# Performance work log

Hardware: AMD Instinct MI355X
Metric: run time of the kernel (lower is better)

Reference implementation:

```python
import jax, jax.numpy as jnp
import numpy as np

B = 2048   # batch
C = 64     # EEG channels (num_eegch)
T = 125    # time samples -> pool5 -> 25 -> (p=5, 5)
H = 8      # num_heads
L = 6      # num_layers
D = 16     # num_projected_features
QK = 8     # qkv_len
P = 5      # tokens before cls
EPS = 1e-5


def setup_inputs() -> dict:
    key = jax.random.key(0)
    ks = iter(jax.random.split(key, 64))

    def nrm(shape, s=0.05):
        return jax.random.normal(next(ks), shape, jnp.float32) * s

    return {
        "x": jax.random.normal(next(ks), (B, 1, C, T), jnp.float32),
        "conv_t_w": nrm((8, 1, 1, 63)),
        "conv_t_b": nrm((8,)),
        "bn1_g": 1.0 + nrm((8,)),
        "bn1_b": nrm((8,)),
        "bn1_m": nrm((8,)),
        "bn1_v": 1.0 + 0.1 * jax.random.uniform(next(ks), (8,), jnp.float32),
        "conv_s_w": nrm((16, 1, C, 1)),
        "conv_s_b": nrm((16,)),
        "bn2_g": 1.0 + nrm((16,)),
        "bn2_b": nrm((16,)),
        "bn2_m": nrm((16,)),
        "bn2_v": 1.0 + 0.1 * jax.random.uniform(next(ks), (16,), jnp.float32),
        "proj_w": nrm((D, 16 * 5)),
        "proj_b": nrm((D,)),
        "cls_token": nrm((1, 1, D), 1.0),
        "pe": nrm((1, P + 1, D), 1.0),
        "qkv_w": nrm((L, 3 * H * QK, D)),
        "qkv_b": nrm((L, 3 * H * QK)),
        "out_w": nrm((L, D, H * QK)),
        "out_b": nrm((L, D)),
        "ln1_g": jnp.ones((L, D), jnp.float32),
        "ln1_b": jnp.zeros((L, D), jnp.float32),
        "ln2_g": jnp.ones((L, D), jnp.float32),
        "ln2_b": jnp.zeros((L, D), jnp.float32),
        "mlp_w1": nrm((L, 2 * D, D)),
        "mlp_b1": nrm((L, 2 * D)),
        "mlp_w2": nrm((L, D, 2 * D)),
        "mlp_b2": nrm((L, D)),
        "head_ln_g": jnp.ones((D,), jnp.float32),
        "head_ln_b": jnp.zeros((D,), jnp.float32),
        "head_w": nrm((2, D)),
        "head_b": nrm((2,)),
    }


def _bn(z, g, b, m, v):
    s = (g * jax.lax.rsqrt(v + EPS))[None, :, None, None]
    return (z - m[None, :, None, None]) * s + b[None, :, None, None]


def _ln(z, g, b):
    m = z.mean(-1, keepdims=True)
    var = jnp.mean((z - m) ** 2, -1, keepdims=True)
    return (z - m) * jax.lax.rsqrt(var + EPS) * g + b


def _forward(x, conv_t_w, conv_t_b, bn1_g, bn1_b, bn1_m, bn1_v,
             conv_s_w, conv_s_b, bn2_g, bn2_b, bn2_m, bn2_v,
             proj_w, proj_b, cls_token, pe,
             qkv_w, qkv_b, out_w, out_b, ln1_g, ln1_b, ln2_g, ln2_b,
             mlp_w1, mlp_b1, mlp_w2, mlp_b2,
             head_ln_g, head_ln_b, head_w, head_b):
    b = x.shape[0]
    dn = ('NCHW', 'OIHW', 'NCHW')
    # temporal conv, 'same' padding on width (kernel 63 -> pad 31/31)
    y = jax.lax.conv_general_dilated(x, conv_t_w, (1, 1), [(0, 0), (31, 31)], dimension_numbers=dn)
    y = _bn(y + conv_t_b[None, :, None, None], bn1_g, bn1_b, bn1_m, bn1_v)
    # grouped spatial conv collapses the EEG-channel axis
    y = jax.lax.conv_general_dilated(y, conv_s_w, (1, 1), 'VALID', dimension_numbers=dn, feature_group_count=8)
    y = _bn(y + conv_s_b[None, :, None, None], bn2_g, bn2_b, bn2_m, bn2_v)
    y = jax.nn.elu(y)                              # (b,16,1,125)
    y = y.reshape(b, 16, 1, T // 5, 5).mean(-1)    # avg_pool2d (1,5) -> (b,16,1,25)
    # dropout: identity at inference
    y = y.reshape(b, 16, 1, P, 5)
    y = jnp.swapaxes(y, 3, 4)
    tok = jnp.swapaxes(y.reshape(b, 16 * 5, P), 1, 2)   # (b,5,80)
    tok = tok @ proj_w.T + proj_b                       # (b,5,16)
    z = jnp.concatenate([jnp.broadcast_to(cls_token, (b, 1, D)), tok], axis=1) + pe  # (b,6,16)
    scale = QK ** -0.5
    for i in range(L):
        h1 = _ln(z, ln1_g[i], ln1_b[i])
        qkv = h1 @ qkv_w[i].T + qkv_b[i]                # (b,6,3*H*QK)
        q, k, v = jnp.split(qkv, 3, axis=-1)
        q = q.reshape(b, P + 1, H, QK).transpose(0, 2, 1, 3)
        k = k.reshape(b, P + 1, H, QK).transpose(0, 2, 1, 3)
        v = v.reshape(b, P + 1, H, QK).transpose(0, 2, 1, 3)
        att = jax.nn.softmax(jnp.einsum('bhsd,bhtd->bhst', q, k) * scale, axis=-1)
        o = jnp.einsum('bhst,bhtd->bhsd', att, v).transpose(0, 2, 1, 3).reshape(b, P + 1, H * QK)
        z = o @ out_w[i].T + out_b[i] + z
        h2 = _ln(z, ln2_g[i], ln2_b[i])
        m = jax.nn.gelu(h2 @ mlp_w1[i].T + mlp_b1[i], approximate=False) @ mlp_w2[i].T + mlp_b2[i]
        z = m + z
    cls = _ln(z[:, 0, :], head_ln_g, head_ln_b)
    return jax.nn.softmax(cls @ head_w.T + head_b, axis=-1)


def reference(x, conv_t_w, conv_t_b, bn1_g, bn1_b, bn1_m, bn1_v,
              conv_s_w, conv_s_b, bn2_g, bn2_b, bn2_m, bn2_v,
              proj_w, proj_b, cls_token, pe,
              qkv_w, qkv_b, out_w, out_b, ln1_g, ln1_b, ln2_g, ln2_b,
              mlp_w1, mlp_b1, mlp_w2, mlp_b2,
              head_ln_g, head_ln_b, head_w, head_b):
    return _forward(x, conv_t_w, conv_t_b, bn1_g, bn1_b, bn1_m, bn1_v,
                    conv_s_w, conv_s_b, bn2_g, bn2_b, bn2_m, bn2_v,
                    proj_w, proj_b, cls_token, pe,
                    qkv_w, qkv_b, out_w, out_b, ln1_g, ln1_b, ln2_g, ln2_b,
                    mlp_w1, mlp_b1, mlp_w2, mlp_b2,
                    head_ln_g, head_ln_b, head_w, head_b)
```

## Files before the change

kernel.cpp:

```cpp
#include <hip/hip_runtime.h>

#define WAVE_SYNC() do { asm volatile("" ::: "memory"); \
                         __builtin_amdgcn_wave_barrier(); \
                         asm volatile("" ::: "memory"); } while (0)

typedef _Float16 h2 __attribute__((ext_vector_type(2)));
typedef _Float16 h4 __attribute__((ext_vector_type(4)));
typedef _Float16 h8 __attribute__((ext_vector_type(8)));

__device__ __forceinline__ float fdot2(h2 a, h2 b, float c) {
#if defined(__has_builtin)
#if __has_builtin(__builtin_amdgcn_fdot2)
    return __builtin_amdgcn_fdot2(a, b, c, false);
#else
    return (float)a[0]*(float)b[0] + (float)a[1]*(float)b[1] + c;
#endif
#else
    return (float)a[0]*(float)b[0] + (float)a[1]*(float)b[1] + c;
#endif
}

__device__ __forceinline__ float dot8h(h8 a, h8 b, float c) {
    float s = c;
    #pragma unroll
    for (int i = 0; i < 4; ++i) {
        h2 x = {a[2*i], a[2*i+1]};
        h2 y = {b[2*i], b[2*i+1]};
        s = fdot2(x, y, s);
    }
    return s;
}

__device__ __forceinline__ float dot16h(h8 a0, h8 a1, h8 b0, h8 b1, float c) {
    return dot8h(a1, b1, dot8h(a0, b0, c));
}

__device__ __forceinline__ float ln_norm16(float z, float g, float bb) {
    float s = z, q = z * z;
    #pragma unroll
    for (int off = 8; off >= 1; off >>= 1) {
        s += __shfl_xor(s, off, 16);
        q += __shfl_xor(q, off, 16);
    }
    float mean = s * 0.0625f;
    float var  = q * 0.0625f - mean * mean;
    return (z - mean) * rsqrtf(var + 1e-5f) * g + bb;
}

__device__ __forceinline__ float gelu_exact(float a) {
    float xa = fabsf(a) * 0.70710678118654752f;
    float tt = 1.f / (1.f + 0.3275911f * xa);
    float poly = tt * (0.254829592f + tt * (-0.284496736f + tt * (1.421413741f
               + tt * (-1.453152027f + tt * 1.061405429f))));
    float erfv = 1.f - poly * __expf(-xa * xa);
    erfv = a >= 0.f ? erfv : -erfv;
    return 0.5f * a * (1.f + erfv);
}

#define F_XSTR 204
#define F_PL   4000
#define F_TOT  4448

extern "C" __global__ __launch_bounds__(64, 2)
void eegnet_frontend(
    const float* __restrict__ x,
    const float* __restrict__ conv_t_w, const float* __restrict__ conv_t_b,
    const float* __restrict__ bn1_g, const float* __restrict__ bn1_b,
    const float* __restrict__ bn1_m, const float* __restrict__ bn1_v,
    const float* __restrict__ conv_s_w, const float* __restrict__ conv_s_b,
    const float* __restrict__ bn2_g, const float* __restrict__ bn2_b,
    const float* __restrict__ bn2_m, const float* __restrict__ bn2_v,
    const float* __restrict__ proj_w, const float* __restrict__ proj_b,
    float* __restrict__ tokws)
{
    __shared__ __align__(16) float sm[F_TOT];
    _Float16* xr = reinterpret_cast<_Float16*>(sm);
    const int b    = blockIdx.x;
    const int lane = threadIdx.x;

    {
        const float4* xb4 = reinterpret_cast<const float4*>(x + (size_t)b * 8000);
        #pragma unroll
        for (int k = 0; k < 32; ++k) {
            int g = min(k * 64 + lane, 1999);
            float4 v = xb4[g];
            h4 hv = {(_Float16)v.x, (_Float16)v.y, (_Float16)v.z, (_Float16)v.w};
            *reinterpret_cast<h4*>(&xr[4 * g]) = hv;
        }
    }
    WAVE_SYNC();

    {
        const int l2 = min(lane, 60);
        float a0[16], a1[16];
        #pragma unroll
        for (int o = 0; o < 16; ++o) { a0[o] = 0.f; a1[o] = 0.f; }
        #pragma unroll 8
        for (int c = 0; c < 64; ++c) {
            float xv0 = (float)xr[c * 125 + lane];
            float xv1 = (float)xr[c * 125 + 64 + l2];
            #pragma unroll
            for (int o = 0; o < 16; ++o) {
                float w = conv_s_w[o * 64 + c];
                a0[o] += w * xv0;
                a1[o] += w * xv1;
            }
        }
        WAVE_SYNC();

        for (int i = lane; i < 16 * 79; i += 64) {
            int row = i / 79, k = i - row * 79;
            int off = (k < 32) ? k : (k + 125);
            sm[row * F_XSTR + off] = 0.f;
        }
        #pragma unroll
        for (int o = 0; o < 16; ++o) {
            sm[o * F_XSTR + 32 + lane] = a0[o];
            if (lane < 61) sm[o * F_XSTR + 96 + lane] = a1[o];
        }
    }

    const int oo = lane & 15, qg = lane >> 4, gg = oo >> 1;
    float sa, cc;
    {
        float s1 = bn1_g[gg] * rsqrtf(bn1_v[gg] + 1e-5f);
        float b1 = (conv_t_b[gg] - bn1_m[gg]) * s1 + bn1_b[gg];
        float s2 = bn2_g[oo] * rsqrtf(bn2_v[oo] + 1e-5f);
        float ssum = 0.f;
        const float4* csw = reinterpret_cast<const float4*>(conv_s_w + oo * 64);
        #pragma unroll
        for (int i = 0; i < 16; ++i) {
            float4 v = csw[i];
            ssum += v.x + v.y + v.z + v.w;
        }
        sa = s1 * s2;
        cc = (b1 * ssum + conv_s_b[oo] - bn2_m[oo]) * s2 + bn2_b[oo];
    }
    float wt[63];
    #pragma unroll
    for (int k = 0; k < 63; ++k) wt[k] = conv_t_w[gg * 63 + k];

    WAVE_SYNC();

    #pragma unroll 2
    for (int jj = 0; jj < 7; ++jj) {
        int j  = qg * 7 + jj;
        int jc = min(j, 24);
        int base = oo * F_XSTR + 5 * jc + 1;
        float acc5[5] = {0.f, 0.f, 0.f, 0.f, 0.f};
        #pragma unroll
        for (int m = 0; m < 67; ++m) {
            float xv = sm[base + m];
            #pragma unroll
            for (int u = 0; u < 5; ++u)
                if (u <= m && m - u <= 62) acc5[u] += wt[m - u] * xv;
        }
        float psum = 0.f;
        #pragma unroll
        for (int u = 0; u < 5; ++u) {
            float v = acc5[u] * sa + cc;
            psum += (v > 0.f) ? v : (__expf(v) - 1.f);
        }
        if (j == jc) sm[F_PL + oo * 28 + j] = psum * 0.2f;
    }

    WAVE_SYNC();

    #pragma unroll
    for (int pass = 0; pass < 2; ++pass) {
        int oi = (pass == 0) ? lane : (64 + lane);
        int p = oi >> 4, dd = oi & 15;
        int pc = min(p, 4);
        bool act = (pass == 0) || (lane < 16);
        float acc = proj_b[dd];
        const float4* wp = reinterpret_cast<const float4*>(proj_w + dd * 80);
        #pragma unroll
        for (int i = 0; i < 20; ++i) {
            float4 w4 = wp[i];
            acc += w4.x * sm[F_PL + ((4*i+0)/5) * 28 + pc * 5 + ((4*i+0)%5)];
            acc += w4.y * sm[F_PL + ((4*i+1)/5) * 28 + pc * 5 + ((4*i+1)%5)];
            acc += w4.z * sm[F_PL + ((4*i+2)/5) * 28 + pc * 5 + ((4*i+2)%5)];
            acc += w4.w * sm[F_PL + ((4*i+3)/5) * 28 + pc * 5 + ((4*i+3)%5)];
        }
        if (act) tokws[b * 80 + pc * 16 + dd] = acc;
    }
}

#define WQKVH 0
#define WOUTH 4608
#define WM1H  5760
#define WM2H  6528
#define BQKVF 3584
#define BOUTF 3776
#define BM1F  3792
#define BM2F  3824
#define LN1GF 3840
#define LN1BF 3856
#define LN2GF 3872
#define LN2BF 3888
#define SCR0  7808
#define SSTRH 1584
#define SH1H  0
#define SQKVH 144
#define SMHSH 1344
#define T_BYTES 28288

extern "C" __global__ __launch_bounds__(256, 2)
void eegnet_transformer(
    const float* __restrict__ cls_token, const float* __restrict__ pe,
    const float* __restrict__ qkv_w, const float* __restrict__ qkv_b,
    const float* __restrict__ out_w, const float* __restrict__ out_b,
    const float* __restrict__ ln1_g, const float* __restrict__ ln1_b,
    const float* __restrict__ ln2_g, const float* __restrict__ ln2_b,
    const float* __restrict__ mlp_w1, const float* __restrict__ mlp_b1,
    const float* __restrict__ mlp_w2, const float* __restrict__ mlp_b2,
    const float* __restrict__ head_ln_g, const float* __restrict__ head_ln_b,
    const float* __restrict__ head_w, const float* __restrict__ head_b,
    const float* __restrict__ tokws, float* __restrict__ out)
{
    __shared__ __align__(16) unsigned char smb[T_BYTES];
    float*    smf = reinterpret_cast<float*>(smb);
    _Float16* smh = reinterpret_cast<_Float16*>(smb);

    const int tid = threadIdx.x;
    const int ss  = tid >> 7;
    const int u   = tid & 127;
    const int sA  = blockIdx.x * 4 + ss * 2;
    const int d16 = u & 15, qg = u >> 4;
    const int t6c = min(qg, 5);
    const int wav = u >> 6, al = u & 63;
    const int sbA = SCR0 + (ss * 2    ) * SSTRH;
    const int sbB = SCR0 + (ss * 2 + 1) * SSTRH;

    float zA, zB;
    {
        float peV = pe[t6c * 16 + d16];
        if (t6c == 0) {
            float cv = cls_token[d16];
            zA = cv + peV; zB = cv + peV;
        } else {
            zA = tokws[(sA    ) * 80 + (t6c - 1) * 16 + d16] + peV;
            zB = tokws[(sA + 1) * 80 + (t6c - 1) * 16 + d16] + peV;
        }
    }

    #pragma unroll 1
    for (int li = 0; li < 6; ++li) {
        __syncthreads();

        {
            const float4* s1 = reinterpret_cast<const float4*>(qkv_w + li * 3072);
            #pragma unroll
            for (int it = 0; it < 3; ++it) {
                int i = tid + it * 256;
                float4 v = s1[i];
                int j = i >> 2, k = (i & 3) << 2;
                h4 hv = {(_Float16)v.x, (_Float16)v.y, (_Float16)v.z, (_Float16)v.w};
                *reinterpret_cast<h4*>(&smh[WQKVH + j * 24 + k]) = hv;
            }
            {
                float4 v = reinterpret_cast<const float4*>(out_w + li * 1024)[tid];
                int j = tid >> 4, k = (tid & 15) << 2;
                h4 hv = {(_Float16)v.x, (_Float16)v.y, (_Float16)v.z, (_Float16)v.w};
                *reinterpret_cast<h4*>(&smh[WOUTH + j * 72 + k]) = hv;
            }
            if (tid < 128) {
                float4 v = reinterpret_cast<const float4*>(mlp_w1 + li * 512)[tid];
                int j = tid >> 2, k = (tid & 3) << 2;
                h4 hv = {(_Float16)v.x, (_Float16)v.y, (_Float16)v.z, (_Float16)v.w};
                *reinterpret_cast<h4*>(&smh[WM1H + j * 24 + k]) = hv;
            } else {
                int i = tid - 128;
                float4 v = reinterpret_cast<const float4*>(mlp_w2 + li * 512)[i];
                int j = i >> 3, k = (i & 7) << 2;
                h4 hv = {(_Float16)v.x, (_Float16)v.y, (_Float16)v.z, (_Float16)v.w};
                *reinterpret_cast<h4*>(&smh[WM2H + j * 40 + k]) = hv;
            }
            if (tid < 192) smf[BQKVF + tid] = qkv_b[li * 192 + tid];
            else if (tid < 208) smf[BOUTF + tid - 192] = out_b[li * 16 + tid - 192];
            else if (tid < 240) smf[BM1F + tid - 208]  = mlp_b1[li * 32 + tid - 208];
            else               smf[BM2F + tid - 240]  = mlp_b2[li * 16 + tid - 240];
            if (tid >= 64 && tid < 80)        smf[LN1GF + tid - 64]  = ln1_g[li * 16 + tid - 64];
            else if (tid >= 80 && tid < 96)   smf[LN1BF + tid - 80]  = ln1_b[li * 16 + tid - 80];
            else if (tid >= 96 && tid < 112)  smf[LN2GF + tid - 96]  = ln2_g[li * 16 + tid - 96];
            else if (tid >= 112 && tid < 128) smf[LN2BF + tid - 112] = ln2_b[li * 16 + tid - 112];
        }
        __syncthreads();

        {
            float g = smf[LN1GF + d16], bb = smf[LN1BF + d16];
            smh[sbA + SH1H + t6c * 24 + d16] = (_Float16)ln_norm16(zA, g, bb);
            smh[sbB + SH1H + t6c * 24 + d16] = (_Float16)ln_norm16(zB, g, bb);
        }
        WAVE_SYNC();

        h8 hA0 = *reinterpret_cast<const h8*>(&smh[sbA + SH1H + t6c * 24]);
        h8 hA1 = *reinterpret_cast<const h8*>(&smh[sbA + SH1H + t6c * 24 + 8]);
        h8 hB0 = *reinterpret_cast<const h8*>(&smh[sbB + SH1H + t6c * 24]);
        h8 hB1 = *reinterpret_cast<const h8*>(&smh[sbB + SH1H + t6c * 24 + 8]);

        #pragma unroll 2
        for (int r = 0; r < 12; ++r) {
            int j = d16 + 16 * r;
            h8 w0 = *reinterpret_cast<const h8*>(&smh[WQKVH + j * 24]);
            h8 w1 = *reinterpret_cast<const h8*>(&smh[WQKVH + j * 24 + 8]);
            float bb = smf[BQKVF + j];
            smh[sbA + SQKVH + t6c * 200 + j] = (_Float16)dot16h(hA0, hA1, w0, w1, bb);
            smh[sbB + SQKVH + t6c * 200 + j] = (_Float16)dot16h(hB0, hB1, w0, w1, bb);
        }
        __syncthreads();

        {
            bool act = (wav == 0) ? (al < 32) : (al < 16);
            if (act) {
                int h  = al & 7;
                int qs = (wav == 0) ? (al >> 3) : 4 + (al >> 3);
                const int qoffA = sbA + SQKVH + qs * 200 + h * 8;
                const int qoffB = sbB + SQKVH + qs * 200 + h * 8;
                h8 qA = *reinterpret_cast<const h8*>(&smh[qoffA]);
                h8 qB = *reinterpret_cast<const h8*>(&smh[qoffB]);
                float scA[6], scB[6];
                #pragma unroll
                for (int t = 0; t < 6; ++t) {
                    h8 kA = *reinterpret_cast<const h8*>(&smh[sbA + SQKVH + t * 200 + 64 + h * 8]);
                    h8 kB = *reinterpret_cast<const h8*>(&smh[sbB + SQKVH + t * 200 + 64 + h * 8]);
                    scA[t] = dot8h(qA, kA, 0.f) * 0.35355339059327373f;
                    scB[t] = dot8h(qB, kB, 0.f) * 0.35355339059327373f;
                }
                float mxA = scA[0], mxB = scB[0];
                #pragma unroll
                for (int t = 1; t < 6; ++t) { mxA = fmaxf(mxA, scA[t]); mxB = fmaxf(mxB, scB[t]); }
                float suA = 0.f, suB = 0.f;
                #pragma unroll
                for (int t = 0; t < 6; ++t) {
                    scA[t] = __expf(scA[t] - mxA); suA += scA[t];
                    scB[t] = __expf(scB[t] - mxB); suB += scB[t];
                }
                float ivA = 1.f / suA, ivB = 1.f / suB;
                h2 oA[4], oB[4];
                #pragma unroll
                for (int k2 = 0; k2 < 4; ++k2) { oA[k2] = h2{0, 0}; oB[k2] = h2{0, 0}; }
                #pragma unroll
                for (int t = 0; t < 6; ++t) {
                    h8 vA = *reinterpret_cast<const h8*>(&smh[sbA + SQKVH + t * 200 + 128 + h * 8]);
                    h8 vB = *reinterpret_cast<const h8*>(&smh[sbB + SQKVH + t * 200 + 128 + h * 8]);
                    _Float16 aa = (_Float16)(scA[t] * ivA);
                    _Float16 ab = (_Float16)(scB[t] * ivB);
                    h2 av = {aa, aa}, bv = {ab, ab};
                    #pragma unroll
                    for (int k2 = 0; k2 < 4; ++k2) {
                        h2 va = {vA[2*k2], vA[2*k2+1]};
                        h2 vb = {vB[2*k2], vB[2*k2+1]};
                        oA[k2] += av * va;
                        oB[k2] += bv * vb;
                    }
                }
                h8 stA, stB;
                #pragma unroll
                for (int k2 = 0; k2 < 4; ++k2) {
                    stA[2*k2] = oA[k2][0]; stA[2*k2+1] = oA[k2][1];
                    stB[2*k2] = oB[k2][0]; stB[2*k2+1] = oB[k2][1];
                }
                *reinterpret_cast<h8*>(&smh[qoffA]) = stA;
                *reinterpret_cast<h8*>(&smh[qoffB]) = stB;
            }
        }
        WAVE_SYNC();

        {
            float aA = smf[BOUTF + d16], aB = aA;
            #pragma unroll
            for (int i = 0; i < 8; ++i) {
                h8 w  = *reinterpret_cast<const h8*>(&smh[WOUTH + d16 * 72 + 8 * i]);
                h8 va = *reinterpret_cast<const h8*>(&smh[sbA + SQKVH + t6c * 200 + 8 * i]);
                h8 vb = *reinterpret_cast<const h8*>(&smh[sbB + SQKVH + t6c * 200 + 8 * i]);
                aA = dot8h(va, w, aA);
                aB = dot8h(vb, w, aB);
            }
            zA += aA; zB += aB;
        }

        {
            float g = smf[LN2GF + d16], bb = smf[LN2BF + d16];
            smh[sbA + SH1H + t6c * 24 + d16] = (_Float16)ln_norm16(zA, g, bb);
            smh[sbB + SH1H + t6c * 24 + d16] = (_Float16)ln_norm16(zB, g, bb);
        }
        WAVE_SYNC();
        hA0 = *reinterpret_cast<const h8*>(&smh[sbA + SH1H + t6c * 24]);
        hA1 = *reinterpret_cast<const h8*>(&smh[sbA + SH1H + t6c * 24 + 8]);
        hB0 = *reinterpret_cast<const h8*>(&smh[sbB + SH1H + t6c * 24]);
        hB1 = *reinterpret_cast<const h8*>(&smh[sbB + SH1H + t6c * 24 + 8]);

        #pragma unroll
        for (int r = 0; r < 2; ++r) {
            int uu = d16 + 16 * r;
            h8 w0 = *reinterpret_cast<const h8*>(&smh[WM1H + uu * 24]);
            h8 w1 = *reinterpret_cast<const h8*>(&smh[WM1H + uu * 24 + 8]);
            float bb = smf[BM1F + uu];
            float aA = dot16h(hA0, hA1, w0, w1, bb);
            float aB = dot16h(hB0, hB1, w0, w1, bb);
            smh[sbA + SMHSH + t6c * 40 + uu] = (_Float16)gelu_exact(aA);
            smh[sbB + SMHSH + t6c * 40 + uu] = (_Float16)gelu_exact(aB);
        }
        WAVE_SYNC();

        {
            float aA = smf[BM2F + d16], aB = aA;
            #pragma unroll
            for (int i = 0; i < 4; ++i) {
                h8 w  = *reinterpret_cast<const h8*>(&smh[WM2H + d16 * 40 + 8 * i]);
                h8 va = *reinterpret_cast<const h8*>(&smh[sbA + SMHSH + t6c * 40 + 8 * i]);
                h8 vb = *reinterpret_cast<const h8*>(&smh[sbB + SMHSH + t6c * 40 + 8 * i]);
                aA = dot8h(va, w, aA);
                aB = dot8h(vb, w, aB);
            }
            zA += aA; zB += aB;
        }
    }

    if (u < 16) {
        float g = head_ln_g[d16], bb = head_ln_b[d16];
        float w0 = head_w[d16], w1 = head_w[16 + d16];
        float cvA = ln_norm16(zA, g, bb);
        float cvB = ln_norm16(zB, g, bb);
        float pA0 = cvA * w0, pA1 = cvA * w1;
        float pB0 = cvB * w0, pB1 = cvB * w1;
        #pragma unroll
        for (int off = 8; off >= 1; off >>= 1) {
            pA0 += __shfl_xor(pA0, off, 16);
            pA1 += __shfl_xor(pA1, off, 16);
            pB0 += __shfl_xor(pB0, off, 16);
            pB1 += __shfl_xor(pB1, off, 16);
        }
        if (u == 0) {
            float hb0 = head_b[0], hb1 = head_b[1];
            {
                float l0 = pA0 + hb0, l1 = pA1 + hb1;
                float mx = fmaxf(l0, l1);
                float e0 = __expf(l0 - mx), e1 = __expf(l1 - mx);
                float inv = 1.f / (e0 + e1);
                out[sA * 2 + 0] = e0 * inv;
                out[sA * 2 + 1] = e1 * inv;
            }
            {
                float l0 = pB0 + hb0, l1 = pB1 + hb1;
                float mx = fmaxf(l0, l1);
                float e0 = __expf(l0 - mx), e1 = __expf(l1 - mx);
                float inv = 1.f / (e0 + e1);
                out[(sA + 1) * 2 + 0] = e0 * inv;
                out[(sA + 1) * 2 + 1] = e1 * inv;
            }
        }
    }
}

extern "C" void kernel_launch(void* const* d_in, const int* in_sizes, int n_in,
                              void* d_out, int out_size, void* d_ws, size_t ws_size,
                              hipStream_t stream) {
    (void)n_in; (void)ws_size; (void)out_size;
    const float* a0  = (const float*)d_in[0];
    const float* a1  = (const float*)d_in[1];
    const float* a2  = (const float*)d_in[2];
    const float* a3  = (const float*)d_in[3];
    const float* a4  = (const float*)d_in[4];
    const float* a5  = (const float*)d_in[5];
    const float* a6  = (const float*)d_in[6];
    const float* a7  = (const float*)d_in[7];
    const float* a8  = (const float*)d_in[8];
    const float* a9  = (const float*)d_in[9];
    const float* a10 = (const float*)d_in[10];
    const float* a11 = (const float*)d_in[11];
    const float* a12 = (const float*)d_in[12];
    const float* a13 = (const float*)d_in[13];
    const float* a14 = (const float*)d_in[14];
    const float* a15 = (const float*)d_in[15];
    const float* a16 = (const float*)d_in[16];
    const float* a17 = (const float*)d_in[17];
    const float* a18 = (const float*)d_in[18];
    const float* a19 = (const float*)d_in[19];
    const float* a20 = (const float*)d_in[20];
    const float* a21 = (const float*)d_in[21];
    const float* a22 = (const float*)d_in[22];
    const float* a23 = (const float*)d_in[23];
    const float* a24 = (const float*)d_in[24];
    const float* a25 = (const float*)d_in[25];
    const float* a26 = (const float*)d_in[26];
    const float* a27 = (const float*)d_in[27];
    const float* a28 = (const float*)d_in[28];
    const float* a29 = (const float*)d_in[29];
    const float* a30 = (const float*)d_in[30];
    const float* a31 = (const float*)d_in[31];
    const float* a32 = (const float*)d_in[32];

    int Bn = in_sizes[0] / (64 * 125);
    float* tokws = (float*)d_ws;

    eegnet_frontend<<<Bn, 64, 0, stream>>>(
        a0, a1, a2, a3, a4, a5, a6, a7, a8, a9, a10, a11, a12, a13, a14, tokws);

    eegnet_transformer<<<Bn / 4, 256, 0, stream>>>(
        a15, a16, a17, a18, a19, a20, a21, a22, a23, a24, a25, a26, a27, a28,
        a29, a30, a31, a32, tokws, (float*)d_out);
}
```

Baseline: 217.1 us.

## Restructure EEG frontend to 128 threads with per-time spatial conv and fp16 LDS

The frontend kernel moves from one 64-thread wave to two waves per sample. Each of the first 125 threads now owns a time column and computes all 16 spatial-conv outputs straight from global memory, with no fp16 staging pass for the input. The spatial-conv outputs are kept in LDS as fp16, which halves shared memory use and allows more resident blocks. In exchange it needs block barriers instead of wave barriers, leaves some lanes idle, and puts 64 strided global loads per thread into registers, which may raise register pressure.

```diff
diff --git a/kernel.cpp b/kernel.cpp
--- a/kernel.cpp
+++ b/kernel.cpp
@@ -57,11 +57,11 @@
     return 0.5f * a * (1.f + erfv);
 }
 
-#define F_XSTR 204
-#define F_PL   4000
-#define F_TOT  4448
-
-extern "C" __global__ __launch_bounds__(64, 2)
+#define FS_XSTR 210
+#define FS_PF   1680
+#define FS_TOTF 2128
+
+extern "C" __global__ __launch_bounds__(128, 4)
 void eegnet_frontend(
     const float* __restrict__ x,
     const float* __restrict__ conv_t_w, const float* __restrict__ conv_t_b,
@@ -73,54 +73,35 @@
     const float* __restrict__ proj_w, const float* __restrict__ proj_b,
     float* __restrict__ tokws)
 {
-    __shared__ __align__(16) float sm[F_TOT];
-    _Float16* xr = reinterpret_cast<_Float16*>(sm);
-    const int b    = blockIdx.x;
-    const int lane = threadIdx.x;
-
-    {
-        const float4* xb4 = reinterpret_cast<const float4*>(x + (size_t)b * 8000);
-        #pragma unroll
-        for (int k = 0; k < 32; ++k) {
-            int g = min(k * 64 + lane, 1999);
-            float4 v = xb4[g];
-            h4 hv = {(_Float16)v.x, (_Float16)v.y, (_Float16)v.z, (_Float16)v.w};
-            *reinterpret_cast<h4*>(&xr[4 * g]) = hv;
-        }
-    }
-    WAVE_SYNC();
-
-    {
-        const int l2 = min(lane, 60);
-        float a0[16], a1[16];
-        #pragma unroll
-        for (int o = 0; o < 16; ++o) { a0[o] = 0.f; a1[o] = 0.f; }
-        #pragma unroll 8
-        for (int c = 0; c < 64; ++c) {
-            float xv0 = (float)xr[c * 125 + lane];
-            float xv1 = (float)xr[c * 125 + 64 + l2];
+    __shared__ __align__(16) float sm[FS_TOTF];
+    _Float16* smh = reinterpret_cast<_Float16*>(sm);
+    const int b   = blockIdx.x;
+    const int tid = threadIdx.x;
+
+    for (int i = tid; i < 16 * 85; i += 128) {
+        int row = i / 85, k = i - row * 85;
+        int off = (k < 32) ? k : (k + 125);
+        smh[row * FS_XSTR + off] = (_Float16)0.f;
+    }
+
+    if (tid < 125) {
+        const float* xb = x + (size_t)b * 8000 + tid;
+        float xc[64];
+        #pragma unroll
+        for (int c = 0; c < 64; ++c) xc[c] = xb[c * 125];
+        #pragma unroll
+        for (int o = 0; o < 16; ++o) {
+            const float* wr = conv_s_w + o * 64;
+            float acc = 0.f;
             #pragma unroll
-            for (int o = 0; o < 16; ++o) {
-                float w = conv_s_w[o * 64 + c];
-                a0[o] += w * xv0;
-                a1[o] += w * xv1;
-            }
-        }
-        WAVE_SYNC();
-
-        for (int i = lane; i < 16 * 79; i += 64) {
-            int row = i / 79, k = i - row * 79;
-            int off = (k < 32) ? k : (k + 125);
-            sm[row * F_XSTR + off] = 0.f;
-        }
-        #pragma unroll
-        for (int o = 0; o < 16; ++o) {
-            sm[o * F_XSTR + 32 + lane] = a0[o];
-            if (lane < 61) sm[o * F_XSTR + 96 + lane] = a1[o];
-        }
-    }
-
-    const int oo = lane & 15, qg = lane >> 4, gg = oo >> 1;
+            for (int c = 0; c < 64; ++c) acc += wr[c] * xc[c];
+            smh[o * FS_XSTR + 32 + tid] = (_Float16)acc;
+        }
+    }
+
+    __syncthreads();
+
+    const int oo = tid & 15, qg = tid >> 4, gg = oo >> 1;
     float sa, cc;
     {
         float s1 = bn1_g[gg] * rsqrtf(bn1_v[gg] + 1e-5f);
@@ -140,17 +121,15 @@
     #pragma unroll
     for (int k = 0; k < 63; ++k) wt[k] = conv_t_w[gg * 63 + k];
 
-    WAVE_SYNC();
-
     #pragma unroll 2
-    for (int jj = 0; jj < 7; ++jj) {
-        int j  = qg * 7 + jj;
+    for (int jj = 0; jj < 4; ++jj) {
+        int j  = qg * 4 + jj;
         int jc = min(j, 24);
-        int base = oo * F_XSTR + 5 * jc + 1;
+        int base = oo * FS_XSTR + 5 * jc + 1;
         float acc5[5] = {0.f, 0.f, 0.f, 0.f, 0.f};
         #pragma unroll
         for (int m = 0; m < 67; ++m) {
-            float xv = sm[base + m];
+            float xv = (float)smh[base + m];
             #pragma unroll
             for (int u = 0; u < 5; ++u)
                 if (u <= m && m - u <= 62) acc5[u] += wt[m - u] * xv;
@@ -161,28 +140,24 @@
             float v = acc5[u] * sa + cc;
             psum += (v > 0.f) ? v : (__expf(v) - 1.f);
         }
-        if (j == jc) sm[F_PL + oo * 28 + j] = psum * 0.2f;
-    }
-
-    WAVE_SYNC();
-
-    #pragma unroll
-    for (int pass = 0; pass < 2; ++pass) {
-        int oi = (pass == 0) ? lane : (64 + lane);
-        int p = oi >> 4, dd = oi & 15;
-        int pc = min(p, 4);
-        bool act = (pass == 0) || (lane < 16);
+        if (j == jc) sm[FS_PF + oo * 28 + j] = psum * 0.2f;
+    }
+
+    __syncthreads();
+
+    if (tid < 80) {
+        int p = tid >> 4, dd = tid & 15;
         float acc = proj_b[dd];
         const float4* wp = reinterpret_cast<const float4*>(proj_w + dd * 80);
         #pragma unroll
         for (int i = 0; i < 20; ++i) {
             float4 w4 = wp[i];
-            acc += w4.x * sm[F_PL + ((4*i+0)/5) * 28 + pc * 5 + ((4*i+0)%5)];
-            acc += w4.y * sm[F_PL + ((4*i+1)/5) * 28 + pc * 5 + ((4*i+1)%5)];
-            acc += w4.z * sm[F_PL + ((4*i+2)/5) * 28 + pc * 5 + ((4*i+2)%5)];
-            acc += w4.w * sm[F_PL + ((4*i+3)/5) * 28 + pc * 5 + ((4*i+3)%5)];
-        }
-        if (act) tokws[b * 80 + pc * 16 + dd] = acc;
+            acc += w4.x * sm[FS_PF + ((4*i+0)/5) * 28 + p * 5 + ((4*i+0)%5)];
+            acc += w4.y * sm[FS_PF + ((4*i+1)/5) * 28 + p * 5 + ((4*i+1)%5)];
+            acc += w4.z * sm[FS_PF + ((4*i+2)/5) * 28 + p * 5 + ((4*i+2)%5)];
+            acc += w4.w * sm[FS_PF + ((4*i+3)/5) * 28 + p * 5 + ((4*i+3)%5)];
+        }
+        tokws[b * 80 + p * 16 + dd] = acc;
     }
 }
 
@@ -495,7 +470,7 @@
     int Bn = in_sizes[0] / (64 * 125);
     float* tokws = (float*)d_ws;
 
-    eegnet_frontend<<<Bn, 64, 0, stream>>>(
+    eegnet_frontend<<<Bn, 128, 0, stream>>>(
         a0, a1, a2, a3, a4, a5, a6, a7, a8, a9, a10, a11, a12, a13, a14, tokws);
 
     eegnet_transformer<<<Bn / 4, 256, 0, stream>>>(
```

Result: slower. 323.1 us (+48.8%).

## Fuse EEG frontend and transformer into one kernel with two samples per block

Applied to the files above, without the earlier changes.

Merges the convolutional frontend kernel and the transformer kernel into a single kernel. Each 128-thread block has two waves, and each wave runs the frontend for one sample, writing its tokens to shared memory instead of a global workspace. After a block barrier, the transformer processes those two samples. This removes one launch and the global round trip for tokens. In exchange, the transformer now handles two samples per block instead of four, so per-layer weight staging happens twice as often relative to the samples processed. The block is also 128 threads wide, which changes occupancy and parallelism.

```diff
diff --git a/kernel.cpp b/kernel.cpp
--- a/kernel.cpp
+++ b/kernel.cpp
@@ -57,134 +57,12 @@
     return 0.5f * a * (1.f + erfv);
 }
 
+
 #define F_XSTR 204
 #define F_PL   4000
 #define F_TOT  4448
-
-extern "C" __global__ __launch_bounds__(64, 2)
-void eegnet_frontend(
-    const float* __restrict__ x,
-    const float* __restrict__ conv_t_w, const float* __restrict__ conv_t_b,
-    const float* __restrict__ bn1_g, const float* __restrict__ bn1_b,
-    const float* __restrict__ bn1_m, const float* __restrict__ bn1_v,
-    const float* __restrict__ conv_s_w, const float* __restrict__ conv_s_b,
-    const float* __restrict__ bn2_g, const float* __restrict__ bn2_b,
-    const float* __restrict__ bn2_m, const float* __restrict__ bn2_v,
-    const float* __restrict__ proj_w, const float* __restrict__ proj_b,
-    float* __restrict__ tokws)
-{
-    __shared__ __align__(16) float sm[F_TOT];
-    _Float16* xr = reinterpret_cast<_Float16*>(sm);
-    const int b    = blockIdx.x;
-    const int lane = threadIdx.x;
-
-    {
-        const float4* xb4 = reinterpret_cast<const float4*>(x + (size_t)b * 8000);
-        #pragma unroll
-        for (int k = 0; k < 32; ++k) {
-            int g = min(k * 64 + lane, 1999);
-            float4 v = xb4[g];
-            h4 hv = {(_Float16)v.x, (_Float16)v.y, (_Float16)v.z, (_Float16)v.w};
-            *reinterpret_cast<h4*>(&xr[4 * g]) = hv;
-        }
-    }
-    WAVE_SYNC();
-
-    {
-        const int l2 = min(lane, 60);
-        float a0[16], a1[16];
-        #pragma unroll
-        for (int o = 0; o < 16; ++o) { a0[o] = 0.f; a1[o] = 0.f; }
-        #pragma unroll 8
-        for (int c = 0; c < 64; ++c) {
-            float xv0 = (float)xr[c * 125 + lane];
-            float xv1 = (float)xr[c * 125 + 64 + l2];
-            #pragma unroll
-            for (int o = 0; o < 16; ++o) {
-                float w = conv_s_w[o * 64 + c];
-                a0[o] += w * xv0;
-                a1[o] += w * xv1;
-            }
-        }
-        WAVE_SYNC();
-
-        for (int i = lane; i < 16 * 79; i += 64) {
-            int row = i / 79, k = i - row * 79;
-            int off = (k < 32) ? k : (k + 125);
-            sm[row * F_XSTR + off] = 0.f;
-        }
-        #pragma unroll
-        for (int o = 0; o < 16; ++o) {
-            sm[o * F_XSTR + 32 + lane] = a0[o];
-            if (lane < 61) sm[o * F_XSTR + 96 + lane] = a1[o];
-        }
-    }
-
-    const int oo = lane & 15, qg = lane >> 4, gg = oo >> 1;
-    float sa, cc;
-    {
-        float s1 = bn1_g[gg] * rsqrtf(bn1_v[gg] + 1e-5f);
-        float b1 = (conv_t_b[gg] - bn1_m[gg]) * s1 + bn1_b[gg];
-        float s2 = bn2_g[oo] * rsqrtf(bn2_v[oo] + 1e-5f);
-        float ssum = 0.f;
-        const float4* csw = reinterpret_cast<const float4*>(conv_s_w + oo * 64);
-        #pragma unroll
-        for (int i = 0; i < 16; ++i) {
-            float4 v = csw[i];
-            ssum += v.x + v.y + v.z + v.w;
-        }
-        sa = s1 * s2;
-        cc = (b1 * ssum + conv_s_b[oo] - bn2_m[oo]) * s2 + bn2_b[oo];
-    }
-    float wt[63];
-    #pragma unroll
-    for (int k = 0; k < 63; ++k) wt[k] = conv_t_w[gg * 63 + k];
-
-    WAVE_SYNC();
-
-    #pragma unroll 2
-    for (int jj = 0; jj < 7; ++jj) {
-        int j  = qg * 7 + jj;
-        int jc = min(j, 24);
-        int base = oo * F_XSTR + 5 * jc + 1;
-        float acc5[5] = {0.f, 0.f, 0.f, 0.f, 0.f};
-        #pragma unroll
-        for (int m = 0; m < 67; ++m) {
-            float xv = sm[base + m];
-            #pragma unroll
-            for (int u = 0; u < 5; ++u)
-                if (u <= m && m - u <= 62) acc5[u] += wt[m - u] * xv;
-        }
-        float psum = 0.f;
-        #pragma unroll
-        for (int u = 0; u < 5; ++u) {
-            float v = acc5[u] * sa + cc;
-            psum += (v > 0.f) ? v : (__expf(v) - 1.f);
-        }
-        if (j == jc) sm[F_PL + oo * 28 + j] = psum * 0.2f;
-    }
-
-    WAVE_SYNC();
-
-    #pragma unroll
-    for (int pass = 0; pass < 2; ++pass) {
-        int oi = (pass == 0) ? lane : (64 + lane);
-        int p = oi >> 4, dd = oi & 15;
-        int pc = min(p, 4);
-        bool act = (pass == 0) || (lane < 16);
-        float acc = proj_b[dd];
-        const float4* wp = reinterpret_cast<const float4*>(proj_w + dd * 80);
-        #pragma unroll
-        for (int i = 0; i < 20; ++i) {
-            float4 w4 = wp[i];
-            acc += w4.x * sm[F_PL + ((4*i+0)/5) * 28 + pc * 5 + ((4*i+0)%5)];
-            acc += w4.y * sm[F_PL + ((4*i+1)/5) * 28 + pc * 5 + ((4*i+1)%5)];
-            acc += w4.z * sm[F_PL + ((4*i+2)/5) * 28 + pc * 5 + ((4*i+2)%5)];
-            acc += w4.w * sm[F_PL + ((4*i+3)/5) * 28 + pc * 5 + ((4*i+3)%5)];
-        }
-        if (act) tokws[b * 80 + pc * 16 + dd] = acc;
-    }
-}
+#define TOKF   8896
+#define FUSED_TOTF 9056
 
 #define WQKVH 0
 #define WOUTH 4608
@@ -203,10 +81,17 @@
 #define SH1H  0
 #define SQKVH 144
 #define SMHSH 1344
-#define T_BYTES 28288
-
-extern "C" __global__ __launch_bounds__(256, 2)
-void eegnet_transformer(
+
+extern "C" __global__ __launch_bounds__(128, 2)
+void eegnet_fused(
+    const float* __restrict__ x,
+    const float* __restrict__ conv_t_w, const float* __restrict__ conv_t_b,
+    const float* __restrict__ bn1_g, const float* __restrict__ bn1_b,
+    const float* __restrict__ bn1_m, const float* __restrict__ bn1_v,
+    const float* __restrict__ conv_s_w, const float* __restrict__ conv_s_b,
+    const float* __restrict__ bn2_g, const float* __restrict__ bn2_b,
+    const float* __restrict__ bn2_m, const float* __restrict__ bn2_v,
+    const float* __restrict__ proj_w, const float* __restrict__ proj_b,
     const float* __restrict__ cls_token, const float* __restrict__ pe,
     const float* __restrict__ qkv_w, const float* __restrict__ qkv_b,
     const float* __restrict__ out_w, const float* __restrict__ out_b,
@@ -216,21 +101,136 @@
     const float* __restrict__ mlp_w2, const float* __restrict__ mlp_b2,
     const float* __restrict__ head_ln_g, const float* __restrict__ head_ln_b,
     const float* __restrict__ head_w, const float* __restrict__ head_b,
-    const float* __restrict__ tokws, float* __restrict__ out)
+    float* __restrict__ out)
 {
-    __shared__ __align__(16) unsigned char smb[T_BYTES];
-    float*    smf = reinterpret_cast<float*>(smb);
-    _Float16* smh = reinterpret_cast<_Float16*>(smb);
-
-    const int tid = threadIdx.x;
-    const int ss  = tid >> 7;
-    const int u   = tid & 127;
-    const int sA  = blockIdx.x * 4 + ss * 2;
-    const int d16 = u & 15, qg = u >> 4;
+    __shared__ __align__(16) float sm[FUSED_TOTF];
+    _Float16* smh = reinterpret_cast<_Float16*>(sm);
+
+    const int tid  = threadIdx.x;
+    const int lane = tid & 63;
+    const int w    = tid >> 6;
+    const int b    = blockIdx.x * 2 + w;
+
+    {
+        float* smw = sm + w * F_TOT;
+        _Float16* xr = reinterpret_cast<_Float16*>(smw);
+
+        {
+            const float4* xb4 = reinterpret_cast<const float4*>(x + (size_t)b * 8000);
+            #pragma unroll
+            for (int k = 0; k < 32; ++k) {
+                int g = min(k * 64 + lane, 1999);
+                float4 v = xb4[g];
+                h4 hv = {(_Float16)v.x, (_Float16)v.y, (_Float16)v.z, (_Float16)v.w};
+                *reinterpret_cast<h4*>(&xr[4 * g]) = hv;
+            }
+        }
+        WAVE_SYNC();
+
+        {
+            const int l2 = min(lane, 60);
+            float a0[16], a1[16];
+            #pragma unroll
+            for (int o = 0; o < 16; ++o) { a0[o] = 0.f; a1[o] = 0.f; }
+            #pragma unroll 8
+            for (int c = 0; c < 64; ++c) {
+                float xv0 = (float)xr[c * 125 + lane];
+                float xv1 = (float)xr[c * 125 + 64 + l2];
+                #pragma unroll
+                for (int o = 0; o < 16; ++o) {
+                    float wv = conv_s_w[o * 64 + c];
+                    a0[o] += wv * xv0;
+                    a1[o] += wv * xv1;
+                }
+            }
+            WAVE_SYNC();
+
+            for (int i = lane; i < 16 * 79; i += 64) {
+                int row = i / 79, k = i - row * 79;
+                int off = (k < 32) ? k : (k + 125);
+                smw[row * F_XSTR + off] = 0.f;
+            }
+            #pragma unroll
+            for (int o = 0; o < 16; ++o) {
+                smw[o * F_XSTR + 32 + lane] = a0[o];
+                if (lane < 61) smw[o * F_XSTR + 96 + lane] = a1[o];
+            }
+        }
+
+        const int oo = lane & 15, qg4 = lane >> 4, gg = oo >> 1;
+        float sa, cc;
+        {
+            float s1 = bn1_g[gg] * rsqrtf(bn1_v[gg] + 1e-5f);
+            float b1 = (conv_t_b[gg] - bn1_m[gg]) * s1 + bn1_b[gg];
+            float s2 = bn2_g[oo] * rsqrtf(bn2_v[oo] + 1e-5f);
+            float ssum = 0.f;
+            const float4* csw = reinterpret_cast<const float4*>(conv_s_w + oo * 64);
+            #pragma unroll
+            for (int i = 0; i < 16; ++i) {
+                float4 v = csw[i];
+                ssum += v.x + v.y + v.z + v.w;
+            }
+            sa = s1 * s2;
+            cc = (b1 * ssum + conv_s_b[oo] - bn2_m[oo]) * s2 + bn2_b[oo];
+        }
+        float wt[63];
+        #pragma unroll
+        for (int k = 0; k < 63; ++k) wt[k] = conv_t_w[gg * 63 + k];
+
+        WAVE_SYNC();
+
+        #pragma unroll 2
+        for (int jj = 0; jj < 7; ++jj) {
+            int j  = qg4 * 7 + jj;
+            int jc = min(j, 24);
+            int base = oo * F_XSTR + 5 * jc + 1;
+            float acc5[5] = {0.f, 0.f, 0.f, 0.f, 0.f};
+            #pragma unroll
+            for (int m = 0; m < 67; ++m) {
+                float xv = smw[base + m];
+                #pragma unroll
+                for (int u = 0; u < 5; ++u)
+                    if (u <= m && m - u <= 62) acc5[u] += wt[m - u] * xv;
+            }
+            float psum = 0.f;
+            #pragma unroll
+            for (int u = 0; u < 5; ++u) {
+                float v = acc5[u] * sa + cc;
+                psum += (v > 0.f) ? v : (__expf(v) - 1.f);
+            }
+            if (j == jc) smw[F_PL + oo * 28 + j] = psum * 0.2f;
+        }
+
+        WAVE_SYNC();
+
+        #pragma unroll
+        for (int pass = 0; pass < 2; ++pass) {
+            int oi = (pass == 0) ? lane : (64 + lane);
+            int p = oi >> 4, dd = oi & 15;
+            int pc = min(p, 4);
+            bool act = (pass == 0) || (lane < 16);
+            float acc = proj_b[dd];
+            const float4* wp = reinterpret_cast<const float4*>(proj_w + dd * 80);
+            #pragma unroll
+            for (int i = 0; i < 20; ++i) {
+                float4 w4 = wp[i];
+                acc += w4.x * smw[F_PL + ((4*i+0)/5) * 28 + pc * 5 + ((4*i+0)%5)];
+                acc += w4.y * smw[F_PL + ((4*i+1)/5) * 28 + pc * 5 + ((4*i+1)%5)];
+                acc += w4.z * smw[F_PL + ((4*i+2)/5) * 28 + pc * 5 + ((4*i+2)%5)];
+                acc += w4.w * smw[F_PL + ((4*i+3)/5) * 28 + pc * 5 + ((4*i+3)%5)];
+            }
+            if (act) sm[TOKF + w * 80 + pc * 16 + dd] = acc;
+        }
+    }
+
+    __syncthreads();
+
+    const int d16 = tid & 15, qg = tid >> 4;
     const int t6c = min(qg, 5);
-    const int wav = u >> 6, al = u & 63;
-    const int sbA = SCR0 + (ss * 2    ) * SSTRH;
-    const int sbB = SCR0 + (ss * 2 + 1) * SSTRH;
+    const int wav = tid >> 6, al = tid & 63;
+    const int sbA = SCR0;
+    const int sbB = SCR0 + SSTRH;
+    const int sA  = blockIdx.x * 2;
 
     float zA, zB;
     {
@@ -239,8 +239,8 @@
             float cv = cls_token[d16];
             zA = cv + peV; zB = cv + peV;
         } else {
-            zA = tokws[(sA    ) * 80 + (t6c - 1) * 16 + d16] + peV;
-            zB = tokws[(sA + 1) * 80 + (t6c - 1) * 16 + d16] + peV;
+            zA = sm[TOKF +      (t6c - 1) * 16 + d16] + peV;
+            zB = sm[TOKF + 80 + (t6c - 1) * 16 + d16] + peV;
         }
     }
 
@@ -251,44 +251,51 @@
         {
             const float4* s1 = reinterpret_cast<const float4*>(qkv_w + li * 3072);
             #pragma unroll
-            for (int it = 0; it < 3; ++it) {
-                int i = tid + it * 256;
+            for (int it = 0; it < 6; ++it) {
+                int i = tid + it * 128;
                 float4 v = s1[i];
                 int j = i >> 2, k = (i & 3) << 2;
                 h4 hv = {(_Float16)v.x, (_Float16)v.y, (_Float16)v.z, (_Float16)v.w};
                 *reinterpret_cast<h4*>(&smh[WQKVH + j * 24 + k]) = hv;
             }
-            {
-                float4 v = reinterpret_cast<const float4*>(out_w + li * 1024)[tid];
-                int j = tid >> 4, k = (tid & 15) << 2;
+            const float4* s2 = reinterpret_cast<const float4*>(out_w + li * 1024);
+            #pragma unroll
+            for (int it = 0; it < 2; ++it) {
+                int i = tid + it * 128;
+                float4 v = s2[i];
+                int j = i >> 4, k = (i & 15) << 2;
                 h4 hv = {(_Float16)v.x, (_Float16)v.y, (_Float16)v.z, (_Float16)v.w};
                 *reinterpret_cast<h4*>(&smh[WOUTH + j * 72 + k]) = hv;
             }
-            if (tid < 128) {
+            {
                 float4 v = reinterpret_cast<const float4*>(mlp_w1 + li * 512)[tid];
                 int j = tid >> 2, k = (tid & 3) << 2;
                 h4 hv = {(_Float16)v.x, (_Float16)v.y, (_Float16)v.z, (_Float16)v.w};
                 *reinterpret_cast<h4*>(&smh[WM1H + j * 24 + k]) = hv;
-            } else {
-                int i = tid - 128;
-                float4 v = reinterpret_cast<const float4*>(mlp_w2 + li * 512)[i];
-                int j = i >> 3, k = (i & 7) << 2;
+            }
+            {
+                float4 v = reinterpret_cast<const float4*>(mlp_w2 + li * 512)[tid];
+                int j = tid >> 3, k = (tid & 7) << 2;
                 h4 hv = {(_Float16)v.x, (_Float16)v.y, (_Float16)v.z, (_Float16)v.w};
                 *reinterpret_cast<h4*>(&smh[WM2H + j * 40 + k]) = hv;
             }
-            if (tid < 192) smf[BQKVF + tid] = qkv_b[li * 192 + tid];
-            else if (tid < 208) smf[BOUTF + tid - 192] = out_b[li * 16 + tid - 192];
-            else if (tid < 240) smf[BM1F + tid - 208]  = mlp_b1[li * 32 + tid - 208];
-            else               smf[BM2F + tid - 240]  = mlp_b2[li * 16 + tid - 240];
-            if (tid >= 64 && tid < 80)        smf[LN1GF + tid - 64]  = ln1_g[li * 16 + tid - 64];
-            else if (tid >= 80 && tid < 96)   smf[LN1BF + tid - 80]  = ln1_b[li * 16 + tid - 80];
-            else if (tid >= 96 && tid < 112)  smf[LN2GF + tid - 96]  = ln2_g[li * 16 + tid - 96];
-            else if (tid >= 112 && tid < 128) smf[LN2BF + tid - 112] = ln2_b[li * 16 + tid - 112];
+            #pragma unroll
+            for (int p = 0; p < 2; ++p) {
+                int i = tid + p * 128;
+                if (i < 192)       sm[BQKVF + i]       = qkv_b[li * 192 + i];
+                else if (i < 208)  sm[BOUTF + i - 192] = out_b[li * 16 + i - 192];
+                else if (i < 240)  sm[BM1F + i - 208]  = mlp_b1[li * 32 + i - 208];
+                else               sm[BM2F + i - 240]  = mlp_b2[li * 16 + i - 240];
+            }
+            if (tid >= 64 && tid < 80)        sm[LN1GF + tid - 64]  = ln1_g[li * 16 + tid - 64];
+            else if (tid >= 80 && tid < 96)   sm[LN1BF + tid - 80]  = ln1_b[li * 16 + tid - 80];
+            else if (tid >= 96 && tid < 112)  sm[LN2GF + tid - 96]  = ln2_g[li * 16 + tid - 96];
+            else if (tid >= 112 && tid < 128) sm[LN2BF + tid - 112] = ln2_b[li * 16 + tid - 112];
         }
         __syncthreads();
 
         {
-            float g = smf[LN1GF + d16], bb = smf[LN1BF + d16];
+            float g = sm[LN1GF + d16], bb = sm[LN1BF + d16];
             smh[sbA + SH1H + t6c * 24 + d16] = (_Float16)ln_norm16(zA, g, bb);
             smh[sbB + SH1H + t6c * 24 + d16] = (_Float16)ln_norm16(zB, g, bb);
         }
@@ -304,7 +311,7 @@
             int j = d16 + 16 * r;
             h8 w0 = *reinterpret_cast<const h8*>(&smh[WQKVH + j * 24]);
             h8 w1 = *reinterpret_cast<const h8*>(&smh[WQKVH + j * 24 + 8]);
-            float bb = smf[BQKVF + j];
+            float bb = sm[BQKVF + j];
             smh[sbA + SQKVH + t6c * 200 + j] = (_Float16)dot16h(hA0, hA1, w0, w1, bb);
             smh[sbB + SQKVH + t6c * 200 + j] = (_Float16)dot16h(hB0, hB1, w0, w1, bb);
         }
@@ -368,20 +375,20 @@
         WAVE_SYNC();
 
         {
-            float aA = smf[BOUTF + d16], aB = aA;
+            float aA = sm[BOUTF + d16], aB = aA;
             #pragma unroll
             for (int i = 0; i < 8; ++i) {
-                h8 w  = *reinterpret_cast<const h8*>(&smh[WOUTH + d16 * 72 + 8 * i]);
+                h8 wv = *reinterpret_cast<const h8*>(&smh[WOUTH + d16 * 72 + 8 * i]);
                 h8 va = *reinterpret_cast<const h8*>(&smh[sbA + SQKVH + t6c * 200 + 8 * i]);
                 h8 vb = *reinterpret_cast<const h8*>(&smh[sbB + SQKVH + t6c * 200 + 8 * i]);
-                aA = dot8h(va, w, aA);
-                aB = dot8h(vb, w, aB);
+                aA = dot8h(va, wv, aA);
+                aB = dot8h(vb, wv, aB);
             }
             zA += aA; zB += aB;
         }
 
         {
-            float g = smf[LN2GF + d16], bb = smf[LN2BF + d16];
+            float g = sm[LN2GF + d16], bb = sm[LN2BF + d16];
             smh[sbA + SH1H + t6c * 24 + d16] = (_Float16)ln_norm16(zA, g, bb);
             smh[sbB + SH1H + t6c * 24 + d16] = (_Float16)ln_norm16(zB, g, bb);
         }
@@ -396,7 +403,7 @@
             int uu = d16 + 16 * r;
             h8 w0 = *reinterpret_cast<const h8*>(&smh[WM1H + uu * 24]);
             h8 w1 = *reinterpret_cast<const h8*>(&smh[WM1H + uu * 24 + 8]);
-            float bb = smf[BM1F + uu];
+            float bb = sm[BM1F + uu];
             float aA = dot16h(hA0, hA1, w0, w1, bb);
             float aB = dot16h(hB0, hB1, w0, w1, bb);
             smh[sbA + SMHSH + t6c * 40 + uu] = (_Float16)gelu_exact(aA);
@@ -405,20 +412,20 @@
         WAVE_SYNC();
 
         {
-            float aA = smf[BM2F + d16], aB = aA;
+            float aA = sm[BM2F + d16], aB = aA;
             #pragma unroll
             for (int i = 0; i < 4; ++i) {
-                h8 w  = *reinterpret_cast<const h8*>(&smh[WM2H + d16 * 40 + 8 * i]);
+                h8 wv = *reinterpret_cast<const h8*>(&smh[WM2H + d16 * 40 + 8 * i]);
                 h8 va = *reinterpret_cast<const h8*>(&smh[sbA + SMHSH + t6c * 40 + 8 * i]);
                 h8 vb = *reinterpret_cast<const h8*>(&smh[sbB + SMHSH + t6c * 40 + 8 * i]);
-                aA = dot8h(va, w, aA);
-                aB = dot8h(vb, w, aB);
+                aA = dot8h(va, wv, aA);
+                aB = dot8h(vb, wv, aB);
             }
             zA += aA; zB += aB;
         }
     }
 
-    if (u < 16) {
+    if (tid < 16) {
         float g = head_ln_g[d16], bb = head_ln_b[d16];
         float w0 = head_w[d16], w1 = head_w[16 + d16];
         float cvA = ln_norm16(zA, g, bb);
@@ -432,7 +439,7 @@
             pB0 += __shfl_xor(pB0, off, 16);
             pB1 += __shfl_xor(pB1, off, 16);
         }
-        if (u == 0) {
+        if (tid == 0) {
             float hb0 = head_b[0], hb1 = head_b[1];
             {
                 float l0 = pA0 + hb0, l1 = pA1 + hb1;
@@ -457,7 +464,7 @@
 extern "C" void kernel_launch(void* const* d_in, const int* in_sizes, int n_in,
                               void* d_out, int out_size, void* d_ws, size_t ws_size,
                               hipStream_t stream) {
-    (void)n_in; (void)ws_size; (void)out_size;
+    (void)n_in; (void)ws_size; (void)out_size; (void)d_ws;
     const float* a0  = (const float*)d_in[0];
     const float* a1  = (const float*)d_in[1];
     const float* a2  = (const float*)d_in[2];
@@ -493,12 +500,9 @@
     const float* a32 = (const float*)d_in[32];
 
     int Bn = in_sizes[0] / (64 * 125);
-    float* tokws = (float*)d_ws;
-
-    eegnet_frontend<<<Bn, 64, 0, stream>>>(
-        a0, a1, a2, a3, a4, a5, a6, a7, a8, a9, a10, a11, a12, a13, a14, tokws);
-
-    eegnet_transformer<<<Bn / 4, 256, 0, stream>>>(
-        a15, a16, a17, a18, a19, a20, a21, a22, a23, a24, a25, a26, a27, a28,
-        a29, a30, a31, a32, tokws, (float*)d_out);
-}
+
+    eegnet_fused<<<Bn / 2, 128, 0, stream>>>(
+        a0, a1, a2, a3, a4, a5, a6, a7, a8, a9, a10, a11, a12,
+        a13, a14, a15, a16, a17, a18, a19, a20, a21, a22, a23, a24,
+        a25, a26, a27, a28, a29, a30, a31, a32, (float*)d_out);
+}
```

Result: no change. 219.0 us (+0.9%).
